# Kernel tuning notes

Hardware: AMD Instinct MI355X
Metric: run time of the kernel (lower is better)

The kernel has to match this reference:

```python
import math
import jax
import jax.numpy as jnp
import numpy as np

N_IMG = 8
A = 3
H = 100
W = 100
STRIDE = 16
IMG = 1600
PRE_NMS_TOP_N = 2000
POST_NMS_TOP_N = 1000
NMS_THRESH = 0.7
MIN_SIZE = 0
BBOX_XFORM_CLIP = math.log(1000.0 / 16.0)


def setup_inputs() -> dict:
    key = jax.random.key(0)
    k1, k2 = jax.random.split(key)
    objectness = jax.random.normal(k1, (N_IMG, A, H, W), jnp.float32)
    box_regression = jax.random.normal(k2, (N_IMG, A * 4, H, W), jnp.float32) * 0.5
    # Grid anchors, flattened in (H, W, A) order to match objectness.permute(0,2,3,1)
    cy = (jnp.arange(H, dtype=jnp.float32) + 0.5) * STRIDE  # [H]
    cx = (jnp.arange(W, dtype=jnp.float32) + 0.5) * STRIDE  # [W]
    half = jnp.array([64.0, 128.0, 256.0], jnp.float32) / 2.0  # [A]
    cy = cy[:, None, None]  # [H,1,1]
    cx = cx[None, :, None]  # [1,W,1]
    s = half[None, None, :]  # [1,1,A]
    x1, y1, x2, y2 = jnp.broadcast_arrays(cx - s, cy - s, cx + s, cy + s)
    anc = jnp.stack([x1, y1, x2, y2], axis=-1).reshape(-1, 4)  # [H*W*A, 4]
    anchors = jnp.broadcast_to(anc[None], (N_IMG, H * W * A, 4)).copy()
    return {
        "objectness": objectness,
        "box_regression": box_regression,
        "anchors": anchors,
        "image_height": IMG,
        "image_width": IMG,
    }


def _decode(deltas, boxes):
    # BoxCoder(weights=(1,1,1,1)).decode with TO_REMOVE=1
    widths = boxes[..., 2] - boxes[..., 0] + 1.0
    heights = boxes[..., 3] - boxes[..., 1] + 1.0
    ctr_x = boxes[..., 0] + 0.5 * widths
    ctr_y = boxes[..., 1] + 0.5 * heights
    dx, dy = deltas[..., 0], deltas[..., 1]
    dw = jnp.minimum(deltas[..., 2], BBOX_XFORM_CLIP)
    dh = jnp.minimum(deltas[..., 3], BBOX_XFORM_CLIP)
    pcx = dx * widths + ctr_x
    pcy = dy * heights + ctr_y
    pw = jnp.exp(dw) * widths
    ph = jnp.exp(dh) * heights
    return jnp.stack(
        [pcx - 0.5 * pw, pcy - 0.5 * ph, pcx + 0.5 * pw - 1.0, pcy + 0.5 * ph - 1.0],
        axis=-1,
    )


def _nms_keep(boxes, valid, thresh):
    # boxes [n,4] sorted by descending score; valid: pre-filter mask.
    n = boxes.shape[0]
    x1, y1, x2, y2 = boxes[:, 0], boxes[:, 1], boxes[:, 2], boxes[:, 3]
    areas = (x2 - x1 + 1.0) * (y2 - y1 + 1.0)
    xx1 = jnp.maximum(x1[:, None], x1[None, :])
    yy1 = jnp.maximum(y1[:, None], y1[None, :])
    xx2 = jnp.minimum(x2[:, None], x2[None, :])
    yy2 = jnp.minimum(y2[:, None], y2[None, :])
    inter = jnp.maximum(xx2 - xx1 + 1.0, 0.0) * jnp.maximum(yy2 - yy1 + 1.0, 0.0)
    iou = inter / (areas[:, None] + areas[None, :] - inter)
    idx = jnp.arange(n)

    def body(i, keep):
        sup = keep[i] & (iou[i] > thresh) & (idx > i)
        return keep & ~sup

    return jax.lax.fori_loop(0, n, body, valid)


def _forward(objectness, box_regression, anchors, image_height, image_width):
    N, A_, H_, W_ = objectness.shape
    scores = jax.nn.sigmoid(objectness.transpose(0, 2, 3, 1).reshape(N, -1))  # [N, A*H*W]
    deltas = (
        box_regression.reshape(N, A_, 4, H_, W_)
        .transpose(0, 3, 4, 1, 2)
        .reshape(N, -1, 4)
    )
    pre = min(PRE_NMS_TOP_N, scores.shape[1])
    top_scores, top_idx = jax.lax.top_k(scores, pre)  # sorted descending
    deltas = jnp.take_along_axis(deltas, top_idx[:, :, None], axis=1)
    anc = jnp.take_along_axis(anchors, top_idx[:, :, None], axis=1)
    props = _decode(deltas, anc)  # [N, pre, 4]
    # clip to image (fact = 1)
    xs = jnp.clip(props[..., 0::2], 0.0, image_width - 1.0)
    ys = jnp.clip(props[..., 1::2], 0.0, image_height - 1.0)
    props = jnp.stack([xs[..., 0], ys[..., 0], xs[..., 1], ys[..., 1]], axis=-1)
    # filter small / out-of-image-center boxes
    ws = props[..., 2] - props[..., 0] + 1.0
    hs = props[..., 3] - props[..., 1] + 1.0
    xc = props[..., 0] + ws / 2.0
    yc = props[..., 1] + hs / 2.0
    valid = (ws >= MIN_SIZE) & (hs >= MIN_SIZE) & (xc < image_width) & (yc < image_height)
    keep = jax.vmap(lambda b, v: _nms_keep(b, v, NMS_THRESH))(props, valid)

    def _select(b, s, k):
        # compact kept boxes (already score-sorted) into fixed-size output
        rank = jnp.cumsum(k) - 1
        tgt = jnp.where(k & (rank < POST_NMS_TOP_N), rank, POST_NMS_TOP_N)
        ob = jnp.zeros((POST_NMS_TOP_N + 1, 4), b.dtype).at[tgt].set(b)[:POST_NMS_TOP_N]
        os = jnp.zeros((POST_NMS_TOP_N + 1,), s.dtype).at[tgt].set(s)[:POST_NMS_TOP_N]
        ov = jnp.arange(POST_NMS_TOP_N) < jnp.minimum(jnp.sum(k), POST_NMS_TOP_N)
        return ob, os, ov

    return jax.vmap(_select)(props, top_scores, keep)


def reference(objectness, box_regression, anchors, image_height, image_width):
    # Returns (boxes [N,post,4], objectness scores [N,post], valid mask [N,post])
    return _forward(objectness, box_regression, anchors, image_height, image_width)
```

## Files before the change

### kernel.cpp

```cpp
#include <hip/hip_runtime.h>
#include <math.h>
#include <stdint.h>

#define NIMG   8
#define NA     30000
#define NQ4    7500
#define PRE_N  2000
#define POST_N 1000
#define NMS_TH 0.7f
#define DCLIP  4.135166556742356f
#define IMGF   1600.0f
#define IMGM1  1599.0f
#define CAND_MAX 4096
#define HPITCH 4104


__device__ __forceinline__ void decode_store(
    uint64_t key, unsigned int rank, int n, const float* __restrict__ breg,
    float* __restrict__ wsBoxes, float* __restrict__ wsScores,
    int* __restrict__ wsValid)
{
    unsigned int idx = (unsigned int)key;
    unsigned int k   = ~((unsigned int)(key >> 32));
    unsigned int u   = (k & 0x80000000u) ? (k & 0x7fffffffu) : ~k;
    float logit = __uint_as_float(u);
    float score = 1.0f / (1.0f + expf(-logit));

    int a = idx % 3, t = idx / 3, w = t % 100, h = t / 100;
    const float* bp = breg + n*120000 + (a*4)*10000 + t;
    float dx = bp[0], dy = bp[10000], dw = bp[20000], dh = bp[30000];

    float half = (a == 0) ? 32.0f : ((a == 1) ? 64.0f : 128.0f);
    float cx = w * 16.0f + 8.0f, cy = h * 16.0f + 8.0f;
    float x1 = cx - half, y1 = cy - half, x2 = cx + half, y2 = cy + half;
    float wd = x2 - x1 + 1.0f, hg = y2 - y1 + 1.0f;
    float cxr = x1 + 0.5f * wd, cyr = y1 + 0.5f * hg;
    dw = fminf(dw, DCLIP); dh = fminf(dh, DCLIP);
    float pcx = dx * wd + cxr, pcy = dy * hg + cyr;
    float pw = expf(dw) * wd, ph = expf(dh) * hg;
    float px1 = pcx - 0.5f * pw, py1 = pcy - 0.5f * ph;
    float px2 = pcx + 0.5f * pw - 1.0f, py2 = pcy + 0.5f * ph - 1.0f;
    px1 = fminf(fmaxf(px1, 0.0f), IMGM1);
    px2 = fminf(fmaxf(px2, 0.0f), IMGM1);
    py1 = fminf(fmaxf(py1, 0.0f), IMGM1);
    py2 = fminf(fmaxf(py2, 0.0f), IMGM1);
    float wss = px2 - px1 + 1.0f, hss = py2 - py1 + 1.0f;
    float xc = px1 + wss * 0.5f, yc = py1 + hss * 0.5f;
    int valid = (wss >= 0.0f) && (hss >= 0.0f) && (xc < IMGF) && (yc < IMGF);

    ((float4*)wsBoxes)[n * PRE_N + (int)rank] = make_float4(px1, py1, px2, py2);
    wsScores[n * PRE_N + (int)rank] = score;
    wsValid [n * PRE_N + (int)rank] = valid;
}

__device__ __forceinline__ unsigned int keyof(float f) {
    unsigned int u = __float_as_uint(f);
    return (u & 0x80000000u) ? ~u : (u | 0x80000000u);
}

__global__ __launch_bounds__(1024) void topk_decode(
    const float* __restrict__ obj, const float* __restrict__ breg,
    float* __restrict__ wsBoxes, float* __restrict__ wsScores,
    int* __restrict__ wsValid)
{
    const int n    = blockIdx.x;
    const int tid  = threadIdx.x;
    const int lane = tid & 63;
    const int wid  = tid >> 6;
    const int rep  = wid & 3;

    __shared__ unsigned int   histf[4 * HPITCH];
    __shared__ unsigned short sufx[4096];
    __shared__ uint64_t       grp[CAND_MAX];
    __shared__ unsigned int   wsum[16];
    __shared__ unsigned int   sbstar;

    for (int b = tid; b < 4 * HPITCH; b += 1024) histf[b] = 0u;
    __syncthreads();

    const float4* obj4 = (const float4*)(obj + n * NA);
    float4 v[8];
    #pragma unroll
    for (int kk = 0; kk < 7; ++kk) v[kk] = obj4[tid + kk * 1024];
    v[7] = make_float4(0.f, 0.f, 0.f, 0.f);
    if (tid < NQ4 - 7 * 1024) v[7] = obj4[tid + 7 * 1024];

    #pragma unroll
    for (int kk = 0; kk < 8; ++kk) {
        if (kk == 7 && tid >= NQ4 - 7 * 1024) continue;
        atomicAdd(&histf[rep * HPITCH + (keyof(v[kk].x) >> 20)], 1u);
        atomicAdd(&histf[rep * HPITCH + (keyof(v[kk].y) >> 20)], 1u);
        atomicAdd(&histf[rep * HPITCH + (keyof(v[kk].z) >> 20)], 1u);
        atomicAdd(&histf[rep * HPITCH + (keyof(v[kk].w) >> 20)], 1u);
    }
    __syncthreads();

    unsigned int c0, c1, c2, c3;
    {
        const int b0 = tid * 4;
        c0 = histf[b0+0] + histf[HPITCH+b0+0] + histf[2*HPITCH+b0+0] + histf[3*HPITCH+b0+0];
        c1 = histf[b0+1] + histf[HPITCH+b0+1] + histf[2*HPITCH+b0+1] + histf[3*HPITCH+b0+1];
        c2 = histf[b0+2] + histf[HPITCH+b0+2] + histf[2*HPITCH+b0+2] + histf[3*HPITCH+b0+2];
        c3 = histf[b0+3] + histf[HPITCH+b0+3] + histf[2*HPITCH+b0+3] + histf[3*HPITCH+b0+3];
    }
    unsigned int p = c0 + c1 + c2 + c3;
    unsigned int s = p;
    #pragma unroll
    for (int off = 1; off < 64; off <<= 1) {
        unsigned int vv = __shfl_down(s, off);
        if (lane + off < 64) s += vv;
    }
    if (lane == 0) wsum[wid] = s;
    __syncthreads();
    unsigned int wafter = 0;
    for (int w = wid + 1; w < 16; ++w) wafter += wsum[w];
    unsigned int after = (s - p) + wafter;
    {
        unsigned int S3 = after + c3;
        unsigned int S2 = S3 + c2;
        unsigned int S1 = S2 + c1;
        unsigned int S0 = S1 + c0;
        if (S3 >= PRE_N && after < PRE_N) { sbstar = tid*4+3; }
        if (S2 >= PRE_N && S3    < PRE_N) { sbstar = tid*4+2; }
        if (S1 >= PRE_N && S2    < PRE_N) { sbstar = tid*4+1; }
        if (S0 >= PRE_N && S1    < PRE_N) { sbstar = tid*4+0; }
        sufx[tid*4+0] = (unsigned short)S1;
        sufx[tid*4+1] = (unsigned short)S2;
        sufx[tid*4+2] = (unsigned short)S3;
        sufx[tid*4+3] = (unsigned short)after;

        const unsigned int st[4] = {S1, S2, S3, after};
        #pragma unroll
        for (int q = 0; q < 4; ++q) {
            const int b = tid*4 + q;
            unsigned int base = st[q];
            #pragma unroll
            for (int r = 0; r < 4; ++r) {
                unsigned int c = histf[r * HPITCH + b];
                histf[r * HPITCH + b] = base;
                base += c;
            }
        }
    }
    __syncthreads();
    const unsigned int bstar = sbstar;

    #pragma unroll
    for (int kk = 0; kk < 8; ++kk) {
        if (kk == 7 && tid >= NQ4 - 7 * 1024) continue;
        const float fv[4] = {v[kk].x, v[kk].y, v[kk].z, v[kk].w};
        #pragma unroll
        for (int e = 0; e < 4; ++e) {
            unsigned int k = keyof(fv[e]);
            unsigned int b = k >> 20;
            if (b < bstar) continue;
            int j = (tid + kk * 1024) * 4 + e;
            int a = j / 10000, t = j - a * 10000;
            uint64_t key = (((uint64_t)(~k)) << 32) | (unsigned int)(t * 3 + a);
            unsigned int slot = atomicAdd(&histf[rep * HPITCH + b], 1u);
            if (slot < CAND_MAX) grp[slot] = key;
        }
    }
    __syncthreads();

    const unsigned int total = min(histf[3 * HPITCH + bstar], (unsigned int)CAND_MAX);

    for (unsigned int slot = tid; slot < total; slot += 1024) {
        const uint64_t key = grp[slot];
        const unsigned int hi = (unsigned int)(key >> 32);
        const unsigned int b  = 4095u - (hi >> 20);
        const unsigned int gbeg = sufx[b];
        const unsigned int gend = min(histf[3 * HPITCH + b], (unsigned int)CAND_MAX);
        unsigned int rank = gbeg;
        unsigned int g = gbeg;
        for (; g + 8u <= gend; g += 8u) {
            uint64_t v0 = grp[g+0], v1 = grp[g+1], v2 = grp[g+2], v3 = grp[g+3];
            uint64_t v4 = grp[g+4], v5 = grp[g+5], v6 = grp[g+6], v7 = grp[g+7];
            unsigned int r0 = (v0 < key) ? 1u : 0u;
            r0 += (v1 < key) ? 1u : 0u;
            r0 += (v2 < key) ? 1u : 0u;
            r0 += (v3 < key) ? 1u : 0u;
            r0 += (v4 < key) ? 1u : 0u;
            r0 += (v5 < key) ? 1u : 0u;
            r0 += (v6 < key) ? 1u : 0u;
            r0 += (v7 < key) ? 1u : 0u;
            rank += r0;
        }
        for (; g < gend; ++g)
            rank += (grp[g] < key) ? 1u : 0u;
        if (rank >= PRE_N) continue;
        decode_store(key, rank, n, breg, wsBoxes, wsScores, wsValid);
    }
}

__global__ __launch_bounds__(512) void nms_mask(
    const float* __restrict__ wsBoxes, uint64_t* __restrict__ mask)
{
    const int blk  = blockIdx.x;
    const int n    = blk >> 5;
    const int i_t  = blk & 31;
    const int tid  = threadIdx.x;
    const int lane = tid & 63;
    const int wv   = tid >> 6;

    __shared__ uint64_t tile[64 * 33];

    for (int idx = tid; idx < 64 * 33; idx += 512) tile[idx] = 0ull;
    __syncthreads();

    const int r = i_t * 64 + lane;
    float4 rb = (r < PRE_N) ? ((const float4*)wsBoxes)[n * PRE_N + r]
                            : make_float4(0.f, 0.f, 0.f, 0.f);
    float ra = (rb.z - rb.x + 1.0f) * (rb.w - rb.y + 1.0f);

    for (int j_t = i_t + wv; j_t < 32; j_t += 8) {
        const int j = j_t * 64 + lane;
        float4 cb = (j < PRE_N) ? ((const float4*)wsBoxes)[n * PRE_N + j]
                                : make_float4(3e30f, 3e30f, 3e30f, 3e30f);
        float ca = (cb.z - cb.x + 1.0f) * (cb.w - cb.y + 1.0f);
        const uint64_t jmask = (j_t == 31) ? 0xFFFFull : ~0ull;
        const bool diag = (j_t == i_t);
        uint64_t myword = 0ull;

        #pragma unroll
        for (int c = 0; c < 64; ++c) {
            float rx1 = __int_as_float(__builtin_amdgcn_readlane(__float_as_int(rb.x), c));
            float ry1 = __int_as_float(__builtin_amdgcn_readlane(__float_as_int(rb.y), c));
            float rx2 = __int_as_float(__builtin_amdgcn_readlane(__float_as_int(rb.z), c));
            float ry2 = __int_as_float(__builtin_amdgcn_readlane(__float_as_int(rb.w), c));
            float rar = __int_as_float(__builtin_amdgcn_readlane(__float_as_int(ra), c));
            float xx1 = fmaxf(rx1, cb.x), yy1 = fmaxf(ry1, cb.y);
            float xx2 = fminf(rx2, cb.z), yy2 = fminf(ry2, cb.w);
            float ww = fmaxf(xx2 - xx1 + 1.0f, 0.0f);
            float hh = fmaxf(yy2 - yy1 + 1.0f, 0.0f);
            float inter = ww * hh;
            float denom = rar + ca - inter;
            unsigned long long bits = __ballot(inter > NMS_TH * denom) & jmask;
            if (diag) bits &= (c == 63) ? 0ull : ((~0ull) << (c + 1));
            if (lane == c) myword = bits;
        }
        tile[lane * 33 + j_t] = myword;
    }
    __syncthreads();

    uint64_t* mrow = mask + ((size_t)n * PRE_N + (size_t)i_t * 64) * 32;
    const int cmax = (i_t == 31) ? 16 : 64;
    for (int idx = tid; idx < cmax * 32; idx += 512) {
        const int rr = idx >> 5, w = idx & 31;
        mrow[idx] = tile[rr * 33 + w];
    }
}

#define SL(n,b) \
    "global_load_dword v" #n ", %[voff], %[sbase]\n\t" \
    "v_add_u32 %[voff], 0x100, %[voff]\n\t"

#define SS(n,b) \
    "s_waitcnt vmcnt(63)\n\t" \
    "v_readlane_b32 %[t], v" #n ", %[lw]\n\t" \
    "s_bitcmp1_b32 %[win], " #b "\n\t" \
    "s_cselect_b32 %[m], 0, -1\n\t" \
    "s_sub_i32 %[kept], %[kept], %[m]\n\t" \
    "s_and_b32 %[t], %[t], %[m]\n\t" \
    "s_or_b32 %[win], %[win], %[t]\n\t" \
    "v_and_b32 v" #n ", %[m], v" #n "\n\t" \
    "v_or_b32 %[rem], %[rem], v" #n "\n\t" \
    "global_load_dword v" #n ", %[voff], %[sbase]\n\t" \
    "v_add_u32 %[voff], 0x100, %[voff]\n\t"

#define SN(n,b,w) \
    "s_waitcnt vmcnt(" #w ")\n\t" \
    "v_readlane_b32 %[t], v" #n ", %[lw]\n\t" \
    "s_bitcmp1_b32 %[win], " #b "\n\t" \
    "s_cselect_b32 %[m], 0, -1\n\t" \
    "s_sub_i32 %[kept], %[kept], %[m]\n\t" \
    "s_and_b32 %[t], %[t], %[m]\n\t" \
    "s_or_b32 %[win], %[win], %[t]\n\t" \
    "v_and_b32 v" #n ", %[m], v" #n "\n\t" \
    "v_or_b32 %[rem], %[rem], v" #n "\n\t"

#define SWIN \
    "s_add_u32 %[lw], %[lw], 1\n\t" \
    "v_readlane_b32 %[t], %[rem], %[lw]\n\t" \
    "s_mov_b32 %[win], %[t]\n\t"

#define ROW_A(M) M(64,0) M(65,1) M(66,2) M(67,3) M(68,4) M(69,5) M(70,6) M(71,7) \
    M(72,8) M(73,9) M(74,10) M(75,11) M(76,12) M(77,13) M(78,14) M(79,15) \
    M(80,16) M(81,17) M(82,18) M(83,19) M(84,20) M(85,21) M(86,22) M(87,23) \
    M(88,24) M(89,25) M(90,26) M(91,27) M(92,28) M(93,29) M(94,30) M(95,31)
#define ROW_B(M) M(96,0) M(97,1) M(98,2) M(99,3) M(100,4) M(101,5) M(102,6) M(103,7) \
    M(104,8) M(105,9) M(106,10) M(107,11) M(108,12) M(109,13) M(110,14) M(111,15) \
    M(112,16) M(113,17) M(114,18) M(115,19) M(116,20) M(117,21) M(118,22) M(119,23) \
    M(120,24) M(121,25) M(122,26) M(123,27) M(124,28) M(125,29) M(126,30) M(127,31)

__global__ __launch_bounds__(256) void nms_scan_select(
    const float* __restrict__ wsBoxes, const float* __restrict__ wsScores,
    const int* __restrict__ wsValid, const uint64_t* __restrict__ mask,
    float* __restrict__ out)
{
    const int n   = blockIdx.x;
    const int tid = threadIdx.x;

    __shared__ __align__(8) unsigned char invb[256];
    __shared__ unsigned int keepw32[64];
    __shared__ int sscan[256];

    unsigned int byte = 0xFFu;
    if (tid < PRE_N / 8) {
        byte = 0u;
        for (int q = 0; q < 8; ++q)
            byte |= (wsValid[n * PRE_N + tid * 8 + q] ? 0u : 1u) << q;
    }
    invb[tid] = (unsigned char)byte;
    __syncthreads();

    if (tid < 64) {
        unsigned int rem = ((const unsigned int*)invb)[tid];
        unsigned long long sbase =
            (unsigned long long)(const void*)(mask + (size_t)n * PRE_N * 32);
        unsigned int voff = (unsigned int)(tid * 4);
        int win_, m_, t_, lw_, kept_, cnt_;

        asm volatile(
            "s_waitcnt vmcnt(0) lgkmcnt(0)\n\t"
            "s_mov_b32 %[kept], 0\n\t"
            "s_mov_b32 %[lw], 0\n\t"
            ROW_A(SL) ROW_B(SL)
            "v_readlane_b32 %[t], %[rem], %[lw]\n\t"
            "s_mov_b32 %[win], %[t]\n\t"
            "s_mov_b32 %[cnt], 30\n\t"
            "Lnms_%=:\n\t"
            ROW_A(SS)
            SWIN
            ROW_B(SS)
            SWIN
            "s_cmp_ge_i32 %[kept], 0x3e8\n\t"
            "s_cbranch_scc1 Lend_%=\n\t"
            "s_sub_u32 %[cnt], %[cnt], 1\n\t"
            "s_cmp_lg_u32 %[cnt], 0\n\t"
            "s_cbranch_scc1 Lnms_%=\n\t"
            SS(64,0) SS(65,1) SS(66,2) SS(67,3) SS(68,4) SS(69,5) SS(70,6) SS(71,7)
            SS(72,8) SS(73,9) SS(74,10) SS(75,11) SS(76,12) SS(77,13) SS(78,14) SS(79,15)
            SN(80,16,63) SN(81,17,62) SN(82,18,61) SN(83,19,60)
            SN(84,20,59) SN(85,21,58) SN(86,22,57) SN(87,23,56)
            SN(88,24,55) SN(89,25,54) SN(90,26,53) SN(91,27,52)
            SN(92,28,51) SN(93,29,50) SN(94,30,49) SN(95,31,48)
            SWIN
            SN(96,0,47) SN(97,1,46) SN(98,2,45) SN(99,3,44)
            SN(100,4,43) SN(101,5,42) SN(102,6,41) SN(103,7,40)
            SN(104,8,39) SN(105,9,38) SN(106,10,37) SN(107,11,36)
            SN(108,12,35) SN(109,13,34) SN(110,14,33) SN(111,15,32)
            SN(112,16,31) SN(113,17,30) SN(114,18,29) SN(115,19,28)
            SN(116,20,27) SN(117,21,26) SN(118,22,25) SN(119,23,24)
            SN(120,24,23) SN(121,25,22) SN(122,26,21) SN(123,27,20)
            SN(124,28,19) SN(125,29,18) SN(126,30,17) SN(127,31,16)
            SWIN
            SN(64,0,15) SN(65,1,14) SN(66,2,13) SN(67,3,12)
            SN(68,4,11) SN(69,5,10) SN(70,6,9) SN(71,7,8)
            SN(72,8,7) SN(73,9,6) SN(74,10,5) SN(75,11,4)
            SN(76,12,3) SN(77,13,2) SN(78,14,1) SN(79,15,0)
            "Lend_%=:\n\t"
            "s_waitcnt vmcnt(0)\n\t"
            : [rem]"+v"(rem), [voff]"+v"(voff),
              [win]"=&s"(win_), [m]"=&s"(m_), [t]"=&s"(t_),
              [lw]"=&s"(lw_), [kept]"=&s"(kept_), [cnt]"=&s"(cnt_)
            : [sbase]"s"(sbase)
            : "scc", "vcc", "memory",
              "v64","v65","v66","v67","v68","v69","v70","v71",
              "v72","v73","v74","v75","v76","v77","v78","v79",
              "v80","v81","v82","v83","v84","v85","v86","v87",
              "v88","v89","v90","v91","v92","v93","v94","v95",
              "v96","v97","v98","v99","v100","v101","v102","v103",
              "v104","v105","v106","v107","v108","v109","v110","v111",
              "v112","v113","v114","v115","v116","v117","v118","v119",
              "v120","v121","v122","v123","v124","v125","v126","v127");

        keepw32[tid] = ~rem;
    }
    __syncthreads();

    int c[8]; const int base8 = tid * 8;
    int lsum = 0;
    for (int q = 0; q < 8; ++q) {
        const int i = base8 + q;
        c[q] = (i < PRE_N) ? (int)((keepw32[i >> 5] >> (i & 31)) & 1u) : 0;
        lsum += c[q];
    }
    sscan[tid] = lsum;
    __syncthreads();
    for (int off = 1; off < 256; off <<= 1) {
        int v = (tid >= off) ? sscan[tid - off] : 0;
        __syncthreads();
        sscan[tid] += v;
        __syncthreads();
    }
    const int excl  = sscan[tid] - lsum;
    const int total = sscan[255];

    float* ob  = out + n * POST_N * 4;
    float* osc = out + NIMG * POST_N * 4 + n * POST_N;
    float* ovd = out + NIMG * POST_N * 5 + n * POST_N;

    for (int i = tid; i < POST_N * 4; i += 256) ob[i] = 0.0f;
    for (int i = tid; i < POST_N; i += 256) osc[i] = 0.0f;
    const int lim = min(total, POST_N);
    for (int i = tid; i < POST_N; i += 256) ovd[i] = (i < lim) ? 1.0f : 0.0f;
    __syncthreads();

    int run = excl;
    for (int q = 0; q < 8; ++q) {
        const int i = base8 + q;
        if (i < PRE_N && c[q]) {
            if (run < POST_N) {
                float4 b = ((const float4*)wsBoxes)[n * PRE_N + i];
                ob[run * 4 + 0] = b.x;
                ob[run * 4 + 1] = b.y;
                ob[run * 4 + 2] = b.z;
                ob[run * 4 + 3] = b.w;
                osc[run] = wsScores[n * PRE_N + i];
            }
            run++;
        }
    }
}

extern "C" void kernel_launch(void* const* d_in, const int* in_sizes, int n_in,
                              void* d_out, int out_size, void* d_ws, size_t ws_size,
                              hipStream_t stream) {
    const float* obj  = (const float*)d_in[0];
    const float* breg = (const float*)d_in[1];
    float* ws        = (float*)d_ws;
    float* wsBoxes   = ws;
    float* wsScores  = ws + 64000;
    int*   wsValid   = (int*)(ws + 80000);
    uint64_t* wsMask = (uint64_t*)(ws + 96000);

    topk_decode<<<NIMG, 1024, 0, stream>>>(obj, breg, wsBoxes, wsScores, wsValid);
    nms_mask<<<NIMG * 32, 512, 0, stream>>>(wsBoxes, wsMask);
    nms_scan_select<<<NIMG, 256, 0, stream>>>(wsBoxes, wsScores, wsValid, wsMask,
                                              (float*)d_out);
}
```

Before: 167.6 us.

## Add second-level radix bucketing for large top-k bins to cut rank comparisons

Candidate bins holding more than 64 keys get a second 8-bit histogram over the next key bits. Their keys are scattered into a new shared buffer grouped by sub-bin, so each key's rank is counted only against its sub-bin rather than the whole bin. This targets the quadratic comparison cost when many logits land in the same top-12-bit bin. It adds extra shared memory, several block barriers and two more passes over the candidates, and it reuses the first-pass histogram storage as scratch.

```diff
diff --git a/kernel.cpp b/kernel.cpp
--- a/kernel.cpp
+++ b/kernel.cpp
@@ -13,6 +13,7 @@
 #define IMGM1  1599.0f
 #define CAND_MAX 4096
 #define HPITCH 4104
+#define BIG_BIN 64
 
 
 __device__ __forceinline__ void decode_store(
@@ -72,8 +73,15 @@
     __shared__ unsigned int   histf[4 * HPITCH];
     __shared__ unsigned short sufx[4096];
     __shared__ uint64_t       grp[CAND_MAX];
+    __shared__ uint64_t       grp2[CAND_MAX];
     __shared__ unsigned int   wsum[16];
     __shared__ unsigned int   sbstar;
+    __shared__ unsigned int   lbbase[16];
+    __shared__ unsigned int   lbcnt, lbtot;
+
+    unsigned int*   hist2  = histf;
+    unsigned short* sufx2  = (unsigned short*)(histf + HPITCH);
+    unsigned char*  bin2lb = (unsigned char*)(histf + 2 * HPITCH);
 
     for (int b = tid; b < 4 * HPITCH; b += 1024) histf[b] = 0u;
     __syncthreads();
@@ -165,29 +173,112 @@
 
     const unsigned int total = min(histf[3 * HPITCH + bstar], (unsigned int)CAND_MAX);
 
+    ((unsigned int*)bin2lb)[tid] = 0xFFFFFFFFu;
+    hist2[tid] = 0u; hist2[tid+1024] = 0u; hist2[tid+2048] = 0u; hist2[tid+3072] = 0u;
+    if (tid == 0) { lbcnt = 0u; lbtot = 0u; }
+    __syncthreads();
+
+    #pragma unroll
+    for (int q = 0; q < 4; ++q) {
+        const unsigned int b = (unsigned int)(tid*4 + q);
+        if (b >= bstar) {
+            const unsigned int ge  = min(histf[3*HPITCH + b], (unsigned int)CAND_MAX);
+            const unsigned int cnt = ge - (unsigned int)sufx[b];
+            if (cnt > (unsigned int)BIG_BIN) {
+                unsigned int pos = atomicAdd(&lbcnt, 1u);
+                if (pos < 16u) {
+                    bin2lb[b] = (unsigned char)pos;
+                    lbbase[pos] = atomicAdd(&lbtot, cnt);
+                }
+            }
+        }
+    }
+    __syncthreads();
+
+    for (unsigned int slot = tid; slot < total; slot += 1024) {
+        const unsigned int hi = (unsigned int)(grp[slot] >> 32);
+        const unsigned int b  = 4095u - (hi >> 20);
+        const unsigned char lb = bin2lb[b];
+        if (lb != 0xFFu)
+            atomicAdd(&hist2[(unsigned int)lb * 256u + ((hi >> 12) & 0xFFu)], 1u);
+    }
+    __syncthreads();
+
+    {
+        const unsigned int nlb = min(lbcnt, 16u);
+        if ((unsigned int)wid < nlb) {
+            const int xb = wid * 256 + lane * 4;
+            unsigned int e0 = hist2[xb+0], e1 = hist2[xb+1],
+                         e2 = hist2[xb+2], e3 = hist2[xb+3];
+            unsigned int tsum = e0 + e1 + e2 + e3;
+            unsigned int inc = tsum;
+            #pragma unroll
+            for (int off = 1; off < 64; off <<= 1) {
+                unsigned int vv = __shfl_up(inc, off);
+                if (lane >= off) inc += vv;
+            }
+            unsigned int base = lbbase[wid] + (inc - tsum);
+            hist2[xb+0] = base;             sufx2[xb+0] = (unsigned short)base;
+            base += e0; hist2[xb+1] = base; sufx2[xb+1] = (unsigned short)base;
+            base += e1; hist2[xb+2] = base; sufx2[xb+2] = (unsigned short)base;
+            base += e2; hist2[xb+3] = base; sufx2[xb+3] = (unsigned short)base;
+        }
+    }
+    __syncthreads();
+
+    for (unsigned int slot = tid; slot < total; slot += 1024) {
+        const uint64_t key = grp[slot];
+        const unsigned int hi = (unsigned int)(key >> 32);
+        const unsigned int b  = 4095u - (hi >> 20);
+        const unsigned char lb = bin2lb[b];
+        if (lb != 0xFFu) {
+            unsigned int d = atomicAdd(&hist2[(unsigned int)lb * 256u + ((hi >> 12) & 0xFFu)], 1u);
+            grp2[d] = key;
+        }
+    }
+    __syncthreads();
+
     for (unsigned int slot = tid; slot < total; slot += 1024) {
         const uint64_t key = grp[slot];
         const unsigned int hi = (unsigned int)(key >> 32);
         const unsigned int b  = 4095u - (hi >> 20);
         const unsigned int gbeg = sufx[b];
         const unsigned int gend = min(histf[3 * HPITCH + b], (unsigned int)CAND_MAX);
-        unsigned int rank = gbeg;
-        unsigned int g = gbeg;
-        for (; g + 8u <= gend; g += 8u) {
-            uint64_t v0 = grp[g+0], v1 = grp[g+1], v2 = grp[g+2], v3 = grp[g+3];
-            uint64_t v4 = grp[g+4], v5 = grp[g+5], v6 = grp[g+6], v7 = grp[g+7];
-            unsigned int r0 = (v0 < key) ? 1u : 0u;
-            r0 += (v1 < key) ? 1u : 0u;
-            r0 += (v2 < key) ? 1u : 0u;
-            r0 += (v3 < key) ? 1u : 0u;
-            r0 += (v4 < key) ? 1u : 0u;
-            r0 += (v5 < key) ? 1u : 0u;
-            r0 += (v6 < key) ? 1u : 0u;
-            r0 += (v7 < key) ? 1u : 0u;
-            rank += r0;
-        }
-        for (; g < gend; ++g)
-            rank += (grp[g] < key) ? 1u : 0u;
+        const unsigned char lb  = bin2lb[b];
+        unsigned int rank;
+
+        if (lb != 0xFFu) {
+            const unsigned int x   = (unsigned int)lb * 256u + ((hi >> 12) & 0xFFu);
+            const unsigned int s2  = sufx2[x];
+            const unsigned int e2v = hist2[x];
+            rank = gbeg + (s2 - lbbase[lb]);
+            for (unsigned int g = s2; g < e2v; g += 8u) {
+                #pragma unroll
+                for (int i = 0; i < 8; ++i) {
+                    const unsigned int gi = g + (unsigned int)i;
+                    const uint64_t vv = grp2[min(gi, e2v - 1u)];
+                    rank += (gi < e2v && vv < key) ? 1u : 0u;
+                }
+            }
+        } else {
+            rank = gbeg;
+            unsigned int g = gbeg;
+            for (; g + 8u <= gend; g += 8u) {
+                uint64_t v0 = grp[g+0], v1 = grp[g+1], v2 = grp[g+2], v3 = grp[g+3];
+                uint64_t v4 = grp[g+4], v5 = grp[g+5], v6 = grp[g+6], v7 = grp[g+7];
+                unsigned int r0 = (v0 < key) ? 1u : 0u;
+                r0 += (v1 < key) ? 1u : 0u;
+                r0 += (v2 < key) ? 1u : 0u;
+                r0 += (v3 < key) ? 1u : 0u;
+                r0 += (v4 < key) ? 1u : 0u;
+                r0 += (v5 < key) ? 1u : 0u;
+                r0 += (v6 < key) ? 1u : 0u;
+                r0 += (v7 < key) ? 1u : 0u;
+                rank += r0;
+            }
+            for (; g < gend; ++g)
+                rank += (grp[g] < key) ? 1u : 0u;
+        }
         if (rank >= PRE_N) continue;
         decode_store(key, rank, n, breg, wsBoxes, wsScores, wsValid);
     }
```

Measured after the change: 154.2 us. -8.0%, faster.
